# Kernel tuning notes

Measured on AMD Instinct MI355X. Metric: run time of the kernel, lower is better.

Reference implementation:

```python
import jax, jax.numpy as jnp
import numpy as np

DIM = 768
NUM_HEADS = 12
HEAD_DIM = DIM // NUM_HEADS
SCALE = HEAD_DIM ** -0.5


def setup_inputs() -> dict:
    key = jax.random.key(0)
    k1, k2, k3, k4 = jax.random.split(key, 4)
    B, N = 8, 1024
    x = jax.random.normal(k1, (B, N, DIM), dtype=jnp.float32)
    # qkv: Linear(dim, 3*dim, bias=False). Stored as [dim, 3*dim] (input-major).
    w_qkv = jax.random.normal(k2, (DIM, 3 * DIM), dtype=jnp.float32) * (DIM ** -0.5)
    # proj: Linear(dim, dim) with bias.
    w_proj = jax.random.normal(k3, (DIM, DIM), dtype=jnp.float32) * (DIM ** -0.5)
    b_proj = jax.random.normal(k4, (DIM,), dtype=jnp.float32) * 0.01
    return {"x": x, "w_qkv": w_qkv, "w_proj": w_proj, "b_proj": b_proj}


def reference(x, w_qkv, w_proj, b_proj):
    B, N, C = x.shape
    H, D = NUM_HEADS, HEAD_DIM
    qkv = (x @ w_qkv).reshape(B, N, 3, H, D)
    qkv = jnp.transpose(qkv, (2, 0, 3, 1, 4))
    q, k, v = qkv[0], qkv[1], qkv[2]
    # attention scores [B, H, N, N]
    attn = jnp.einsum("bhnd,bhmd->bhnm", q, k) * SCALE
    attn = jax.nn.softmax(attn, axis=-1)
    # weighted values -> [B, H, N, D] -> [B, N, C]
    out = jnp.einsum("bhnm,bhmd->bhnd", attn, v)
    out = jnp.transpose(out, (0, 2, 1, 3)).reshape(B, N, C)
    return out @ w_proj + b_proj
```

## Files before the change

kernel.cpp:

```cpp
#include <hip/hip_runtime.h>

#define BATCH 8
#define SEQ   1024
#define DIM   768
#define NH    12
#define HD    64
#define NTOK  (BATCH * SEQ)
#define QKVN  (3 * DIM)
#define QSCALE (0.125f * 1.44269504f)

typedef short bf8   __attribute__((ext_vector_type(8)));
typedef short bf4   __attribute__((ext_vector_type(4)));
typedef float f32x4 __attribute__((ext_vector_type(4)));
typedef int   i32x2 __attribute__((ext_vector_type(2)));
typedef int   i32x4 __attribute__((ext_vector_type(4)));

static __device__ __forceinline__ short f2bf(float f) {
    unsigned u = __float_as_uint(f);
    u += 0x7fffu + ((u >> 16) & 1u);
    return (short)(u >> 16);
}

static __device__ __forceinline__ int pack_bf16(float a, float b) {
    unsigned ua = __float_as_uint(a); ua += 0x7fffu + ((ua >> 16) & 1u);
    unsigned ub = __float_as_uint(b); ub += 0x7fffu + ((ub >> 16) & 1u);
    return (int)((ua >> 16) | (ub & 0xffff0000u));
}

static __device__ __forceinline__ float fast_exp2(float x) {
#if __has_builtin(__builtin_amdgcn_exp2f)
    return __builtin_amdgcn_exp2f(x);
#else
    return exp2f(x);
#endif
}

static __device__ __forceinline__ void gload_lds16(const short* g, short* l) {
    __builtin_amdgcn_global_load_lds(
        (const __attribute__((address_space(1))) void*)g,
        (__attribute__((address_space(3))) void*)l, 16, 0, 0);
}

__global__ __launch_bounds__(256) void convx_k(const float* __restrict__ in,
                                               short* __restrict__ out) {
    int i = blockIdx.x * 256 + threadIdx.x;
    f32x4 v = ((const f32x4*)in)[i];
    bf4 o;
    o[0] = f2bf(v[0]); o[1] = f2bf(v[1]); o[2] = f2bf(v[2]); o[3] = f2bf(v[3]);
    ((bf4*)out)[i] = o;
}

__global__ __launch_bounds__(256) void transpose_bf16_k(
        const float* __restrict__ in, short* __restrict__ out, int R, int C) {
    __shared__ short t[32][33];
    const int tx = threadIdx.x & 31;
    const int ty = threadIdx.x >> 5;
    const int c0 = blockIdx.x * 32;
    const int r0 = blockIdx.y * 32;
    #pragma unroll
    for (int i = 0; i < 32; i += 8)
        t[ty + i][tx] = f2bf(in[(size_t)(r0 + ty + i) * C + c0 + tx]);
    __syncthreads();
    #pragma unroll
    for (int i = 0; i < 32; i += 8)
        out[(size_t)(c0 + ty + i) * R + r0 + tx] = t[tx][ty + i];
}

static __device__ __forceinline__ void gemm_core_128(
        const short* __restrict__ A, const short* __restrict__ WT,
        int m0, int n0, int tid, short* aL, short* bL, f32x4 acc[4][4]) {
    const int lane = tid & 63;
    const int wid  = tid >> 6;
    const int ln   = lane & 15;
    const int quad = lane >> 4;
    const int wm = (wid >> 1) * 64;
    const int wn = (wid & 1) * 64;

    int rowx[4], colx[4];
    #pragma unroll
    for (int cc = 0; cc < 4; cc++) {
        int cf = (wid * 4 + cc) * 64 + lane;
        int r = cf >> 3;
        rowx[cc] = r;
        colx[cc] = (cf & 7) ^ (r & 7);
    }

    for (int kt = 0; kt < DIM; kt += 64) {
        __syncthreads();
        #pragma unroll
        for (int cc = 0; cc < 4; cc++) {
            const int dst = (wid * 4 + cc) * 512;
            gload_lds16(A  + (size_t)(m0 + rowx[cc]) * DIM + kt + colx[cc] * 8, aL + dst);
            gload_lds16(WT + (size_t)(n0 + rowx[cc]) * DIM + kt + colx[cc] * 8, bL + dst);
        }
        __syncthreads();
        #pragma unroll
        for (int kc = 0; kc < 2; kc++) {
            const int sw = ((kc * 4 + quad) ^ (ln & 7)) * 8;
            bf8 af[4], bw[4];
            #pragma unroll
            for (int mi = 0; mi < 4; mi++)
                af[mi] = *(const bf8*)&aL[(wm + mi * 16 + ln) * 64 + sw];
            #pragma unroll
            for (int ni = 0; ni < 4; ni++)
                bw[ni] = *(const bf8*)&bL[(wn + ni * 16 + ln) * 64 + sw];
            #pragma unroll
            for (int mi = 0; mi < 4; mi++)
                #pragma unroll
                for (int ni = 0; ni < 4; ni++)
                    acc[mi][ni] = __builtin_amdgcn_mfma_f32_16x16x32_bf16(
                            af[mi], bw[ni], acc[mi][ni], 0, 0, 0);
        }
    }
}

__global__ __launch_bounds__(256) void gemm_qkv_k(
        const short* __restrict__ X, const short* __restrict__ WT,
        short* __restrict__ Qb, short* __restrict__ Kb, short* __restrict__ VT) {
    __shared__ short aL[128 * 64];
    __shared__ short bL[128 * 64];
    const int tid  = threadIdx.x;
    const int lane = tid & 63;
    const int wid  = tid >> 6;
    const int ln   = lane & 15;
    const int quad = lane >> 4;
    const int m0 = blockIdx.y * 128;
    const int n0 = blockIdx.x * 128;
    const int wm = (wid >> 1) * 64;
    const int wn = (wid & 1) * 64;

    const f32x4 vzero = {0.f, 0.f, 0.f, 0.f};
    f32x4 acc[4][4];
    #pragma unroll
    for (int i = 0; i < 4; i++)
        #pragma unroll
        for (int j = 0; j < 4; j++) acc[i][j] = vzero;

    gemm_core_128(X, WT, m0, n0, tid, aL, bL, acc);

    const int b = m0 / SEQ;
    const int mt = m0 - b * SEQ;
    #pragma unroll
    for (int ni = 0; ni < 4; ni++) {
        const int nb = n0 + wn + ni * 16;
        const int three = nb / DIM;
        const int rem = nb - three * DIM;
        const int h = rem >> 6;
        const int d = (rem & 63) + ln;
        const size_t bh = (size_t)(b * NH + h);
        if (three < 2) {
            short* dst = (three == 0 ? Qb : Kb) + bh * SEQ * HD;
            const float scl = (three == 0) ? QSCALE : 1.0f;
            #pragma unroll
            for (int mi = 0; mi < 4; mi++) {
                #pragma unroll
                for (int r = 0; r < 4; r++) {
                    int tok = mt + wm + mi * 16 + quad * 4 + r;
                    dst[(size_t)tok * HD + d] = f2bf(acc[mi][ni][r] * scl);
                }
            }
        } else {
            short* dst = VT + bh * HD * SEQ + (size_t)d * SEQ;
            #pragma unroll
            for (int mi = 0; mi < 4; mi++) {
                int tok0 = mt + wm + mi * 16 + quad * 4;
                bf4 v;
                v[0] = f2bf(acc[mi][ni][0]); v[1] = f2bf(acc[mi][ni][1]);
                v[2] = f2bf(acc[mi][ni][2]); v[3] = f2bf(acc[mi][ni][3]);
                *(bf4*)&dst[tok0] = v;
            }
        }
    }
}

__global__ __launch_bounds__(256, 3) void attn_k(
        const short* __restrict__ Qb, const short* __restrict__ Kb,
        const short* __restrict__ VT, short* __restrict__ Ob) {
    __shared__ short kL[64 * 64];
    __shared__ short vL[64 * 64];
    const int tid  = threadIdx.x;
    const int lane = tid & 63;
    const int wid  = tid >> 6;
    const int ln   = lane & 15;
    const int quad = lane >> 4;
    const int bh = blockIdx.x;
    const int qt = blockIdx.y;
    const size_t base = (size_t)bh * SEQ * HD;
    const short* qg = Qb + base;
    const short* kg = Kb + base;
    const short* vg = VT + base;
    const int q0 = qt * 128 + wid * 32;

    int srow[2], scol[2];
    #pragma unroll
    for (int cc = 0; cc < 2; cc++) {
        int f = (wid * 2 + cc) * 64 + lane;
        int r = f >> 3;
        srow[cc] = r;
        scol[cc] = (f & 7) ^ (r & 7);
    }

    bf8 bq[2][2];
    #pragma unroll
    for (int qf = 0; qf < 2; qf++)
        #pragma unroll
        for (int kc = 0; kc < 2; kc++)
            bq[qf][kc] = *(const bf8*)&qg[(size_t)(q0 + qf * 16 + ln) * HD + kc * 32 + quad * 8];

    const f32x4 vzero = {0.f, 0.f, 0.f, 0.f};
    f32x4 o[2][4];
    #pragma unroll
    for (int qf = 0; qf < 2; qf++)
        #pragma unroll
        for (int c = 0; c < 4; c++) o[qf][c] = vzero;
    float l_lane[2] = {0.f, 0.f};

    for (int kt = 0; kt < SEQ; kt += 64) {
        __syncthreads();
        #pragma unroll
        for (int cc = 0; cc < 2; cc++) {
            const int dst = (wid * 2 + cc) * 512;
            gload_lds16(kg + (size_t)(kt + srow[cc]) * HD + scol[cc] * 8, kL + dst);
            gload_lds16(vg + (size_t)srow[cc] * SEQ + kt + scol[cc] * 8, vL + dst);
        }
        __syncthreads();

        bf8 ak[4][2];
        #pragma unroll
        for (int ng = 0; ng < 4; ng++)
            #pragma unroll
            for (int kc = 0; kc < 2; kc++)
                ak[ng][kc] = *(const bf8*)&kL[(ng * 16 + ln) * 64 + ((kc * 4 + quad) ^ (ln & 7)) * 8];
        bf8 bv[2][4];
        #pragma unroll
        for (int kch = 0; kch < 2; kch++)
            #pragma unroll
            for (int c = 0; c < 4; c++)
                bv[kch][c] = *(const bf8*)&vL[(c * 16 + ln) * 64 + ((kch * 4 + quad) ^ (ln & 7)) * 8];

        #pragma unroll
        for (int qf = 0; qf < 2; qf++) {
            #pragma unroll
            for (int kch = 0; kch < 2; kch++) {
                f32x4 s0 = __builtin_amdgcn_mfma_f32_16x16x32_bf16(ak[2 * kch][0], bq[qf][0], vzero, 0, 0, 0);
                s0 = __builtin_amdgcn_mfma_f32_16x16x32_bf16(ak[2 * kch][1], bq[qf][1], s0, 0, 0, 0);
                f32x4 s1 = __builtin_amdgcn_mfma_f32_16x16x32_bf16(ak[2 * kch + 1][0], bq[qf][0], vzero, 0, 0, 0);
                s1 = __builtin_amdgcn_mfma_f32_16x16x32_bf16(ak[2 * kch + 1][1], bq[qf][1], s1, 0, 0, 0);

                float e0[4], e1[4];
                #pragma unroll
                for (int r = 0; r < 4; r++) {
                    e0[r] = fast_exp2(s0[r]);
                    e1[r] = fast_exp2(s1[r]);
                    l_lane[qf] += e0[r] + e1[r];
                }
                int P0a = pack_bf16(e0[0], e0[1]);
                int P1a = pack_bf16(e0[2], e0[3]);
                int P0b = pack_bf16(e1[0], e1[1]);
                int P1b = pack_bf16(e1[2], e1[3]);
                i32x2 t0 = __builtin_amdgcn_permlane32_swap(P0a, P0b, false, false);
                i32x2 u0 = __builtin_amdgcn_permlane16_swap(t0[0], t0[1], false, false);
                i32x2 t1 = __builtin_amdgcn_permlane32_swap(P1a, P1b, false, false);
                i32x2 u1 = __builtin_amdgcn_permlane16_swap(t1[0], t1[1], false, false);
                i32x4 ai;
                ai[0] = u0[0]; ai[1] = u1[0]; ai[2] = u0[1]; ai[3] = u1[1];
                bf8 ap = __builtin_bit_cast(bf8, ai);

                #pragma unroll
                for (int c = 0; c < 4; c++)
                    o[qf][c] = __builtin_amdgcn_mfma_f32_16x16x32_bf16(
                            ap, bv[kch][c], o[qf][c], 0, 0, 0);
            }
        }
    }

    const int b = bh / NH;
    const int h = bh - b * NH;
    #pragma unroll
    for (int qf = 0; qf < 2; qf++) {
        float l = l_lane[qf];
        l += __shfl_xor(l, 16, 64);
        l += __shfl_xor(l, 32, 64);
        #pragma unroll
        for (int r = 0; r < 4; r++) {
            float inv = 1.0f / __shfl(l, quad * 4 + r, 64);
            int tok = q0 + qf * 16 + quad * 4 + r;
            size_t off = (size_t)(b * SEQ + tok) * DIM + h * HD;
            #pragma unroll
            for (int c = 0; c < 4; c++)
                Ob[off + c * 16 + ln] = f2bf(o[qf][c][r] * inv);
        }
    }
}

__global__ __launch_bounds__(256) void gemm_proj_k(
        const short* __restrict__ A, const short* __restrict__ WT,
        const float* __restrict__ bias, float* __restrict__ Out) {
    __shared__ short aL[128 * 64];
    __shared__ short bL[128 * 64];
    const int tid  = threadIdx.x;
    const int lane = tid & 63;
    const int ln   = lane & 15;
    const int quad = lane >> 4;
    const int wid  = tid >> 6;
    const int m0 = blockIdx.y * 128;
    const int n0 = blockIdx.x * 128;
    const int wm = (wid >> 1) * 64;
    const int wn = (wid & 1) * 64;

    const f32x4 vzero = {0.f, 0.f, 0.f, 0.f};
    f32x4 acc[4][4];
    #pragma unroll
    for (int i = 0; i < 4; i++)
        #pragma unroll
        for (int j = 0; j < 4; j++) acc[i][j] = vzero;

    gemm_core_128(A, WT, m0, n0, tid, aL, bL, acc);

    #pragma unroll
    for (int ni = 0; ni < 4; ni++) {
        int n = n0 + wn + ni * 16 + ln;
        float bi = bias[n];
        #pragma unroll
        for (int mi = 0; mi < 4; mi++) {
            #pragma unroll
            for (int r = 0; r < 4; r++) {
                int m = m0 + wm + mi * 16 + quad * 4 + r;
                Out[(size_t)m * DIM + n] = acc[mi][ni][r] + bi;
            }
        }
    }
}

extern "C" void kernel_launch(void* const* d_in, const int* in_sizes, int n_in,
                              void* d_out, int out_size, void* d_ws, size_t ws_size,
                              hipStream_t stream) {
    const float* x      = (const float*)d_in[0];
    const float* w_qkv  = (const float*)d_in[1];
    const float* w_proj = (const float*)d_in[2];
    const float* b_proj = (const float*)d_in[3];
    float* out = (float*)d_out;
    char* ws = (char*)d_ws;

    short* wqkvT  = (short*)(ws);
    short* wprojT = (short*)(ws +  3538944);
    short* qb     = (short*)(ws +  4718592);
    short* kb     = (short*)(ws + 17301504);
    short* vt     = (short*)(ws + 29884416);
    short* xb     = (short*)(ws + 42467328);
    short* attn   = xb;

    convx_k<<<dim3(NTOK * DIM / 1024), 256, 0, stream>>>(x, xb);
    transpose_bf16_k<<<dim3(QKVN / 32, DIM / 32), 256, 0, stream>>>(w_qkv, wqkvT, DIM, QKVN);
    transpose_bf16_k<<<dim3(DIM / 32, DIM / 32), 256, 0, stream>>>(w_proj, wprojT, DIM, DIM);
    gemm_qkv_k<<<dim3(QKVN / 128, NTOK / 128), 256, 0, stream>>>(xb, wqkvT, qb, kb, vt);
    attn_k<<<dim3(BATCH * NH, SEQ / 128), 256, 0, stream>>>(qb, kb, vt, attn);
    gemm_proj_k<<<dim3(DIM / 128, NTOK / 128), 256, 0, stream>>>(attn, wprojT, b_proj, out);
}
```

Measured before the change: 198.1 us.

## Double-buffer GEMM LDS tiles and remap blocks for XCD locality

```diff
diff --git a/kernel.cpp b/kernel.cpp
--- a/kernel.cpp
+++ b/kernel.cpp
@@ -85,25 +85,37 @@
         colx[cc] = (cf & 7) ^ (r & 7);
     }
 
-    for (int kt = 0; kt < DIM; kt += 64) {
+    #pragma unroll
+    for (int cc = 0; cc < 4; cc++) {
+        const int dst = (wid * 4 + cc) * 512;
+        gload_lds16(A  + (size_t)(m0 + rowx[cc]) * DIM + colx[cc] * 8, aL + dst);
+        gload_lds16(WT + (size_t)(n0 + rowx[cc]) * DIM + colx[cc] * 8, bL + dst);
+    }
+
+    for (int it = 0; it < DIM / 64; it++) {
+        const int cur = it & 1;
         __syncthreads();
-        #pragma unroll
-        for (int cc = 0; cc < 4; cc++) {
-            const int dst = (wid * 4 + cc) * 512;
-            gload_lds16(A  + (size_t)(m0 + rowx[cc]) * DIM + kt + colx[cc] * 8, aL + dst);
-            gload_lds16(WT + (size_t)(n0 + rowx[cc]) * DIM + kt + colx[cc] * 8, bL + dst);
-        }
-        __syncthreads();
+        if (it + 1 < DIM / 64) {
+            const int nb = (cur ^ 1) * 8192;
+            const int kt = (it + 1) * 64;
+            #pragma unroll
+            for (int cc = 0; cc < 4; cc++) {
+                const int dst = nb + (wid * 4 + cc) * 512;
+                gload_lds16(A  + (size_t)(m0 + rowx[cc]) * DIM + kt + colx[cc] * 8, aL + dst);
+                gload_lds16(WT + (size_t)(n0 + rowx[cc]) * DIM + kt + colx[cc] * 8, bL + dst);
+            }
+        }
+        const int cb = cur * 8192;
         #pragma unroll
         for (int kc = 0; kc < 2; kc++) {
             const int sw = ((kc * 4 + quad) ^ (ln & 7)) * 8;
             bf8 af[4], bw[4];
             #pragma unroll
             for (int mi = 0; mi < 4; mi++)
-                af[mi] = *(const bf8*)&aL[(wm + mi * 16 + ln) * 64 + sw];
+                af[mi] = *(const bf8*)&aL[cb + (wm + mi * 16 + ln) * 64 + sw];
             #pragma unroll
             for (int ni = 0; ni < 4; ni++)
-                bw[ni] = *(const bf8*)&bL[(wn + ni * 16 + ln) * 64 + sw];
+                bw[ni] = *(const bf8*)&bL[cb + (wn + ni * 16 + ln) * 64 + sw];
             #pragma unroll
             for (int mi = 0; mi < 4; mi++)
                 #pragma unroll
@@ -114,18 +126,27 @@
     }
 }
 
+static __device__ __forceinline__ void xcd_map(int id, int NX, int& xt, int& yt) {
+    int r = id % (NX * 8);
+    int g = id / (NX * 8);
+    xt = r >> 3;
+    yt = ((r & 7) << 3) + g;
+}
+
 __global__ __launch_bounds__(256) void gemm_qkv_k(
         const short* __restrict__ X, const short* __restrict__ WT,
         short* __restrict__ Qb, short* __restrict__ Kb, short* __restrict__ VT) {
-    __shared__ short aL[128 * 64];
-    __shared__ short bL[128 * 64];
+    __shared__ short aL[2 * 128 * 64];
+    __shared__ short bL[2 * 128 * 64];
     const int tid  = threadIdx.x;
     const int lane = tid & 63;
     const int wid  = tid >> 6;
     const int ln   = lane & 15;
     const int quad = lane >> 4;
-    const int m0 = blockIdx.y * 128;
-    const int n0 = blockIdx.x * 128;
+    int xt, yt;
+    xcd_map(blockIdx.x, QKVN / 128, xt, yt);
+    const int m0 = yt * 128;
+    const int n0 = xt * 128;
     const int wm = (wid >> 1) * 64;
     const int wn = (wid & 1) * 64;
 
@@ -296,15 +317,17 @@
 __global__ __launch_bounds__(256) void gemm_proj_k(
         const short* __restrict__ A, const short* __restrict__ WT,
         const float* __restrict__ bias, float* __restrict__ Out) {
-    __shared__ short aL[128 * 64];
-    __shared__ short bL[128 * 64];
+    __shared__ short aL[2 * 128 * 64];
+    __shared__ short bL[2 * 128 * 64];
     const int tid  = threadIdx.x;
     const int lane = tid & 63;
     const int ln   = lane & 15;
     const int quad = lane >> 4;
     const int wid  = tid >> 6;
-    const int m0 = blockIdx.y * 128;
-    const int n0 = blockIdx.x * 128;
+    int xt, yt;
+    xcd_map(blockIdx.x, DIM / 128, xt, yt);
+    const int m0 = yt * 128;
+    const int n0 = xt * 128;
     const int wm = (wid >> 1) * 64;
     const int wn = (wid & 1) * 64;
 
@@ -353,7 +376,7 @@
     convx_k<<<dim3(NTOK * DIM / 1024), 256, 0, stream>>>(x, xb);
     transpose_bf16_k<<<dim3(QKVN / 32, DIM / 32), 256, 0, stream>>>(w_qkv, wqkvT, DIM, QKVN);
     transpose_bf16_k<<<dim3(DIM / 32, DIM / 32), 256, 0, stream>>>(w_proj, wprojT, DIM, DIM);
-    gemm_qkv_k<<<dim3(QKVN / 128, NTOK / 128), 256, 0, stream>>>(xb, wqkvT, qb, kb, vt);
+    gemm_qkv_k<<<dim3((QKVN / 128) * (NTOK / 128)), 256, 0, stream>>>(xb, wqkvT, qb, kb, vt);
     attn_k<<<dim3(BATCH * NH, SEQ / 128), 256, 0, stream>>>(qb, kb, vt, attn);
-    gemm_proj_k<<<dim3(DIM / 128, NTOK / 128), 256, 0, stream>>>(attn, wprojT, b_proj, out);
-}
+    gemm_proj_k<<<dim3((DIM / 128) * (NTOK / 128)), 256, 0, stream>>>(attn, wprojT, b_proj, out);
+}
```

Result: faster. 191.6 us (-3.3%).
